# Performance work log

Hardware: AMD Instinct MI355X
Metric: run time of the kernel (lower is better)

## Reference

```python
import jax, jax.numpy as jnp
import numpy as np

N = 32768        # total nodes (B * max_num_nodes)
E = 524288       # edges, avg degree 16
F_ORI = 32       # data.x_ori feature dim
F_G = 32         # each gamora_output feature dim
IN = F_ORI + 3 * F_G  # 128
H = 256          # hidden_dim
OUT = 16         # out_dim
MAXN = 1024      # max_num_nodes
EPS = 1e-5       # BatchNorm eps


def setup_inputs() -> dict:
    key = jax.random.key(0)
    ks = list(jax.random.split(key, 32))
    g = lambda k, shape, fan: jax.random.normal(k, shape, jnp.float32) / np.sqrt(fan)
    inp = {}
    inp['x_ori'] = jax.random.normal(ks[0], (N, F_ORI), jnp.float32)
    inp['g0'] = jax.random.normal(ks[1], (N, F_G), jnp.float32)
    inp['g1'] = jax.random.normal(ks[2], (N, F_G), jnp.float32)
    inp['g2'] = jax.random.normal(ks[3], (N, F_G), jnp.float32)
    inp['edge_index'] = jax.random.randint(ks[4], (2, E), 0, N, jnp.int64)
    # SAGEConv layer 0: in_dim -> hidden
    inp['Wl0'] = g(ks[5], (IN, H), IN)
    inp['Wr0'] = g(ks[6], (IN, H), IN)
    inp['bb0'] = jnp.zeros((H,), jnp.float32)
    # SAGEConv layers 1..3: hidden -> hidden (stacked)
    inp['Wl'] = g(ks[7], (3, H, H), H)
    inp['Wr'] = g(ks[8], (3, H, H), H)
    inp['bb'] = jnp.zeros((3, H), jnp.float32)
    # BatchNorm per conv layer
    inp['gamma'] = jnp.ones((4, H), jnp.float32)
    inp['beta'] = jnp.zeros((4, H), jnp.float32)
    # mlp1: [max_num_nodes, hidden, 1]
    inp['W1a'] = g(ks[9], (MAXN, H), MAXN)
    inp['b1a'] = jnp.zeros((H,), jnp.float32)
    inp['W1b'] = g(ks[10], (H, 1), H)
    inp['b1b'] = jnp.zeros((1,), jnp.float32)
    # final BatchNorm
    inp['gamma_f'] = jnp.ones((H,), jnp.float32)
    inp['beta_f'] = jnp.zeros((H,), jnp.float32)
    # mlp2: [hidden, hidden, out_dim]
    inp['W2a'] = g(ks[11], (H, H), H)
    inp['b2a'] = jnp.zeros((H,), jnp.float32)
    inp['W2b'] = g(ks[12], (H, OUT), H)
    inp['b2b'] = jnp.zeros((OUT,), jnp.float32)
    return inp


def _bn(x, gamma, beta):
    # training-mode BatchNorm1d over the node/batch axis (biased variance)
    m = jnp.mean(x, axis=0)
    v = jnp.var(x, axis=0)
    return (x - m) * jax.lax.rsqrt(v + EPS) * gamma + beta


def _sage(x, src, dst, inv_deg, Wl, Wr, b):
    # mean neighbor aggregation (gather -> segment_sum -> normalize), then
    # out = lin_l(mean_agg) + lin_r(x)  (PyG SAGEConv, aggr='mean')
    agg = jax.ops.segment_sum(x[src], dst, num_segments=N)
    mean = agg * inv_deg[:, None]
    return mean @ Wl + x @ Wr + b


def reference(x_ori, g0, g1, g2, edge_index, Wl0, Wr0, bb0, Wl, Wr, bb,
              gamma, beta, W1a, b1a, W1b, b1b, gamma_f, beta_f,
              W2a, b2a, W2b, b2b):
    x = jnp.concatenate([x_ori, g0, g1, g2], axis=1)  # [N, IN]
    dst, src = edge_index[0], edge_index[1]
    deg = jax.ops.segment_sum(jnp.ones((E,), x.dtype), dst, num_segments=N)
    inv_deg = jnp.where(deg > 0, 1.0 / jnp.maximum(deg, 1.0), 0.0)
    # layer 0
    x = jax.nn.relu(_bn(_sage(x, src, dst, inv_deg, Wl0, Wr0, bb0), gamma[0], beta[0]))
    # layers 1..3 (dropout is identity in eval-mode reference)
    for i in range(3):
        x = jax.nn.relu(_bn(_sage(x, src, dst, inv_deg, Wl[i], Wr[i], bb[i]),
                            gamma[i + 1], beta[i + 1]))
    x = x.reshape(-1, H, MAXN)                 # [B, H, MAXN]
    h = jax.nn.relu(x @ W1a + b1a)             # [B, H, H]
    x = (h @ W1b + b1b).squeeze(2)             # [B, H]
    x = jax.nn.relu(_bn(x, gamma_f, beta_f))
    x = jax.nn.relu(x @ W2a + b2a) @ W2b + b2b  # [B, OUT]
    return x
```

## Files before the change

kernel.cpp:

```cpp
#include <hip/hip_runtime.h>

#define NN 32768
#define NE 524288
#define HD 256
#define TOTP 794897

#define GAS __attribute__((address_space(1)))
#define LAS __attribute__((address_space(3)))

typedef __attribute__((ext_vector_type(8))) __bf16 bf16x8;
typedef __attribute__((ext_vector_type(4))) float f32x4;

__device__ __forceinline__ float ld_any(const void* p, int i, int isbf16) {
    return isbf16 ? (float)((const __bf16*)p)[i] : ((const float*)p)[i];
}

struct PtrTable { const void* p[18]; };


__global__ __launch_bounds__(256) void k_pre(const unsigned* __restrict__ xw, const int* __restrict__ ei,
                                             PtrTable pt, const void* __restrict__ p0, const void* __restrict__ p1,
                                             const void* __restrict__ p2, const void* __restrict__ p3,
                                             int* __restrict__ flags, int* __restrict__ deg,
                                             __bf16* __restrict__ blob, __bf16* __restrict__ X0c) {
    __shared__ int fl[2];
    const int t = threadIdx.x;
    if (t < 64) {
        unsigned L = xw[t] & 0xFFFFu;
        int e = (int)((L >> 7) & 0xFF);
        unsigned long long b = __ballot(e >= 90 && e <= 135);
        if (t == 0) fl[0] = (b == ~0ULL) ? 1 : 0;
    } else if (t < 128) {
        int u = t - 64;
        unsigned long long b = __ballot(ei[2 * u + 1] != 0);
        if (t == 64) fl[1] = (b == 0ULL) ? 1 : 0;
    }
    __syncthreads();
    const int f0 = fl[0], f1 = fl[1];
    const int blk = blockIdx.x;
    if (blk == 0 && t < 2) flags[t] = fl[t];
    if (blk < 2048) {
        int i0 = (blk * 256 + t) * 8;
        int n = i0 >> 7, f = i0 & 127;
        const void* src = (f < 32) ? p0 : (f < 64) ? p1 : (f < 96) ? p2 : p3;
        int si = n * 32 + (f & 31);
        bf16x8 o;
        #pragma unroll
        for (int j = 0; j < 8; ++j) o[j] = (__bf16)ld_any(src, si + j, f0);
        *(bf16x8*)&X0c[i0] = o;
    } else if (blk < 3601) {
        const int off[23] = {0, 32768, 65536, 65792, 131328, 196864, 262400, 327936, 393472,
                             459008, 459776, 460800, 461824, 723968, 724224, 724480, 724481,
                             724737, 724993, 790529, 790785, 794881, TOTP};
        const signed char pidx[22] = {0, 1, 2, 3, 3, 3, 4, 4, 4, 5, 6, 7, 8, 9, 10, 11, 12, 13, 14, 15, 16, 17};
        const int sbase[22] = {0, 0, 0, 0, 65536, 131072, 0, 65536, 131072, 0, 0, 0, 0, 0, 0, 0, 0, 0, 0, 0, 0, 0};
        const signed char lR[22] = {7, 7, -1, 8, 8, 8, 8, 8, 8, -1, -1, -1, 10, -1, -1, -1, -1, -1, -1, -1, -1, -1};
        const signed char lC[22] = {8, 8, 0, 8, 8, 8, 8, 8, 8, 0, 0, 0, 8, 0, 0, 0, 0, 0, 0, 0, 0, 0};
        int base = ((blk - 2048) * 256 + t) * 2;
        #pragma unroll
        for (int j = 0; j < 2; ++j) {
            int i = base + j;
            if (i >= TOTP) break;
            int s = 0;
            while (i >= off[s + 1]) ++s;
            int jj = i - off[s];
            int si;
            if (lR[s] >= 0) {
                int Rm = (1 << lR[s]) - 1;
                si = sbase[s] + ((jj & Rm) << lC[s]) + (jj >> lR[s]);
            } else {
                si = sbase[s] + jj;
            }
            blob[i] = (__bf16)ld_any(pt.p[pidx[s]], si, f0);
        }
    } else {
        int e0 = ((blk - 3601) * 256 + t) * 2;
        int d0 = f1 ? ei[2 * e0] : ei[e0];
        int d1 = f1 ? ei[2 * e0 + 2] : ei[e0 + 1];
        atomicAdd(&deg[d0], 1);
        atomicAdd(&deg[d1], 1);
    }
}


__global__ __launch_bounds__(256) void k_alloc(const int* __restrict__ deg, int* __restrict__ gcur,
                                               int* __restrict__ offs, float* __restrict__ invd) {
    const int n = blockIdx.x * 256 + threadIdx.x;
    const int lane = threadIdx.x & 63;
    const int v = deg[n];
    invd[n] = v ? 1.f / (float)v : 0.f;
    int incl = v;
    #pragma unroll
    for (int d = 1; d < 64; d <<= 1) {
        int y = __shfl_up(incl, d, 64);
        if (lane >= d) incl += y;
    }
    int base = 0;
    if (lane == 63) base = atomicAdd(gcur, incl);
    base = __shfl(base, 63, 64);
    offs[n] = base + incl - v;
}

__global__ __launch_bounds__(256) void k_fill(const int* __restrict__ ei, const int* __restrict__ flags,
                                              const int* __restrict__ offs, int* __restrict__ cursor,
                                              int* __restrict__ csr) {
    int e = blockIdx.x * 256 + threadIdx.x;
    int f = flags[1];
    int d = f ? ei[2 * e] : ei[e];
    int s = f ? ei[2 * NE + 2 * e] : ei[NE + e];
    int p = atomicAdd(&cursor[d], 1);
    csr[offs[d] + p] = s;
}


__global__ __launch_bounds__(256) void k_agg0(const __bf16* __restrict__ X, const int* __restrict__ csr,
                                              const int* __restrict__ offs, const int* __restrict__ deg,
                                              const float* __restrict__ invd, __bf16* __restrict__ M) {
    const int t = threadIdx.x;
    const int s = blockIdx.x & 1;
    const int n = (blockIdx.x >> 1) * 32 + (t >> 3);
    const int fo = s * 64 + (t & 7) * 8;
    const int beg = offs[n], end = beg + deg[n];
    float a[8] = {};
    for (int e = beg; e < end; e += 8) {
        #pragma unroll
        for (int u = 0; u < 8; ++u) {
            int ee = e + u;
            int idx = csr[ee < end ? ee : end - 1] & (NN - 1);
            float mk = ee < end ? 1.f : 0.f;
            bf16x8 v = *(const bf16x8*)&X[(size_t)idx * 128 + fo];
            #pragma unroll
            for (int j = 0; j < 8; ++j) a[j] += mk * (float)v[j];
        }
    }
    const float id = invd[n];
    bf16x8 o;
    #pragma unroll
    for (int j = 0; j < 8; ++j) o[j] = (__bf16)(a[j] * id);
    *(bf16x8*)&M[(size_t)n * 128 + fo] = o;
}

__global__ __launch_bounds__(256) void k_aggq(const unsigned char* __restrict__ Xq, const int* __restrict__ csr,
                                              const int* __restrict__ offs, const int* __restrict__ deg,
                                              const float* __restrict__ invd, __bf16* __restrict__ M) {
    const int t = threadIdx.x;
    const int s = blockIdx.x & 1;
    const int n = (blockIdx.x >> 1) * 32 + (t >> 3);
    const int fo = s * 128 + (t & 7) * 16;
    const int beg = offs[n], end = beg + deg[n];
    unsigned ae0 = 0, ao0 = 0, ae1 = 0, ao1 = 0, ae2 = 0, ao2 = 0, ae3 = 0, ao3 = 0;
    for (int e = beg; e < end; e += 8) {
        #pragma unroll
        for (int u = 0; u < 8; ++u) {
            int ee = e + u;
            int idx = csr[ee < end ? ee : end - 1] & (NN - 1);
            uint4 v = *(const uint4*)&Xq[(size_t)idx * HD + fo];
            if (ee >= end) { v.x = 0u; v.y = 0u; v.z = 0u; v.w = 0u; }
            ae0 += v.x & 0x00FF00FFu; ao0 += (v.x >> 8) & 0x00FF00FFu;
            ae1 += v.y & 0x00FF00FFu; ao1 += (v.y >> 8) & 0x00FF00FFu;
            ae2 += v.z & 0x00FF00FFu; ao2 += (v.z >> 8) & 0x00FF00FFu;
            ae3 += v.w & 0x00FF00FFu; ao3 += (v.w >> 8) & 0x00FF00FFu;
        }
    }
    const float sc = invd[n] * 0.03125f;
    float a[16];
    a[0]  = (float)(ae0 & 0xFFFFu); a[1]  = (float)(ao0 & 0xFFFFu);
    a[2]  = (float)(ae0 >> 16);     a[3]  = (float)(ao0 >> 16);
    a[4]  = (float)(ae1 & 0xFFFFu); a[5]  = (float)(ao1 & 0xFFFFu);
    a[6]  = (float)(ae1 >> 16);     a[7]  = (float)(ao1 >> 16);
    a[8]  = (float)(ae2 & 0xFFFFu); a[9]  = (float)(ao2 & 0xFFFFu);
    a[10] = (float)(ae2 >> 16);     a[11] = (float)(ao2 >> 16);
    a[12] = (float)(ae3 & 0xFFFFu); a[13] = (float)(ao3 & 0xFFFFu);
    a[14] = (float)(ae3 >> 16);     a[15] = (float)(ao3 >> 16);
    bf16x8 o0, o1;
    #pragma unroll
    for (int j = 0; j < 8; ++j) { o0[j] = (__bf16)(a[j] * sc); o1[j] = (__bf16)(a[8 + j] * sc); }
    *(bf16x8*)&M[(size_t)n * HD + fo] = o0;
    *(bf16x8*)&M[(size_t)n * HD + fo + 8] = o1;
}


template <int MODE, int TM, int BNA, int NP, int TN = 128>
__global__ __launch_bounds__(256) void k_gemm(const __bf16* __restrict__ A1, const __bf16* __restrict__ WT1,
                                              const __bf16* __restrict__ A2, const __bf16* __restrict__ WT2,
                                              const __bf16* __restrict__ bias, int KD,
                                              __bf16* __restrict__ O, float* __restrict__ colsum,
                                              const __bf16* __restrict__ W1b, float* __restrict__ x2,
                                              const float* __restrict__ pstatA, const __bf16* __restrict__ gA,
                                              const __bf16* __restrict__ bA) {
    constexpr int NWM = (TN == 128) ? 2 : 4;
    constexpr int MI = TM / (NWM * 16);
    __shared__ __bf16 As[NP][2][TM][32];
    __shared__ __bf16 Bs[NP][2][TN][32];
    __shared__ float scs[256], shs[256];
    const int t = threadIdx.x;
    const int lane = t & 63, w = t >> 6;
    const int wm = (TN == 128) ? (w >> 1) : w;
    const int wn = (TN == 128) ? (w & 1) : 0;
    const int quad = lane >> 4, l15 = lane & 15;
    const int row0 = blockIdx.x * TM, c0 = blockIdx.y * TN;
    const int dr = lane >> 2, dc = (lane & 3) * 8;
    if constexpr (BNA != 0) {
        const float invn = 1.0f / NN;
        float m = pstatA[t] * invn;
        float var = fmaxf(pstatA[256 + t] * invn - m * m, 0.f);
        float rs = rsqrtf(var + 1e-5f);
        float g = (float)gA[t] * rs;
        scs[t] = g;
        shs[t] = (float)bA[t] - m * g;
    }
    f32x4 acc[MI][4] = {};
    for (int k0 = 0; k0 < KD; k0 += 64) {
        __syncthreads();
        #pragma unroll
        for (int pass = 0; pass < NP; ++pass) {
            const __bf16* __restrict__ A = pass ? A2 : A1;
            const __bf16* __restrict__ WT = pass ? WT2 : WT1;
            #pragma unroll
            for (int kk = 0; kk < 2; ++kk) {
                #pragma unroll
                for (int i = 0; i < TN / 64; ++i) {
                    const __bf16* g = &WT[(size_t)(c0 + w * (TN / 4) + i * 16 + dr) * KD + k0 + kk * 32 + dc];
                    __builtin_amdgcn_global_load_lds((const GAS void*)g,
                                                     (LAS void*)&Bs[pass][kk][w * (TN / 4) + i * 16][0], 16, 0, 0);
                }
                if ((BNA >> pass) & 1) {
                    const int kb = (k0 + kk * 32 + dc) & 255;
                    #pragma unroll
                    for (int i = 0; i < TM / 64; ++i) {
                        const __bf16* g = &A[(size_t)(row0 + w * (TM / 4) + i * 16 + dr) * KD + k0 + kk * 32 + dc];
                        bf16x8 v = *(const bf16x8*)g;
                        bf16x8 o;
                        #pragma unroll
                        for (int j = 0; j < 8; ++j)
                            o[j] = (__bf16)fmaxf((float)v[j] * scs[kb + j] + shs[kb + j], 0.f);
                        *(bf16x8*)&As[pass][kk][w * (TM / 4) + i * 16 + dr][dc] = o;
                    }
                } else {
                    #pragma unroll
                    for (int i = 0; i < TM / 64; ++i) {
                        const __bf16* g = &A[(size_t)(row0 + w * (TM / 4) + i * 16 + dr) * KD + k0 + kk * 32 + dc];
                        __builtin_amdgcn_global_load_lds((const GAS void*)g,
                                                         (LAS void*)&As[pass][kk][w * (TM / 4) + i * 16][0],
                                                         16, 0, 0);
                    }
                }
            }
        }
        __syncthreads();
        #pragma unroll
        for (int pass = 0; pass < NP; ++pass) {
            #pragma unroll
            for (int kk = 0; kk < 2; ++kk) {
                bf16x8 af[MI], bfr[4];
                #pragma unroll
                for (int i = 0; i < MI; ++i)
                    af[i] = *(const bf16x8*)&As[pass][kk][wm * (TM / NWM) + i * 16 + l15][quad * 8];
                #pragma unroll
                for (int j = 0; j < 4; ++j)
                    bfr[j] = *(const bf16x8*)&Bs[pass][kk][wn * 64 + j * 16 + l15][quad * 8];
                #pragma unroll
                for (int i = 0; i < MI; ++i)
                    #pragma unroll
                    for (int j = 0; j < 4; ++j)
                        acc[i][j] = __builtin_amdgcn_mfma_f32_16x16x32_bf16(af[i], bfr[j], acc[i][j], 0, 0, 0);
            }
        }
    }
    __syncthreads();
    if constexpr (MODE == 0) {
        float* lsum = (float*)&As[0][0][0][0];
        lsum[t] = 0.f;
        __syncthreads();
        #pragma unroll
        for (int j = 0; j < 4; ++j) {
            const int cb = wn * 64 + j * 16 + l15;
            const int col = c0 + cb;
            const float b = (float)bias[col];
            float s = 0.f, q = 0.f;
            #pragma unroll
            for (int i = 0; i < MI; ++i) {
                const size_t rbase = (size_t)(row0 + wm * (TM / NWM) + i * 16 + quad * 4) * HD + col;
                #pragma unroll
                for (int r = 0; r < 4; ++r) {
                    float y = acc[i][j][r] + b;
                    O[rbase + (size_t)r * HD] = (__bf16)y;
                    s += y;
                    q += y * y;
                }
            }
            s += __shfl_xor(s, 16, 64); s += __shfl_xor(s, 32, 64);
            q += __shfl_xor(q, 16, 64); q += __shfl_xor(q, 32, 64);
            if (quad == 0) {
                atomicAdd(&lsum[cb], s);
                atomicAdd(&lsum[128 + cb], q);
            }
        }
        __syncthreads();
        if (t < 128) atomicAdd(&colsum[c0 + t], lsum[t]);
        else atomicAdd(&colsum[256 + c0 + t - 128], lsum[t]);
    } else {
        float bj[4], wj[4];
        #pragma unroll
        for (int j = 0; j < 4; ++j) {
            const int col = c0 + wn * 64 + j * 16 + l15;
            bj[j] = (float)bias[col];
            wj[j] = (float)W1b[col];
        }
        #pragma unroll
        for (int i = 0; i < MI; ++i) {
            #pragma unroll
            for (int r = 0; r < 4; ++r) {
                float p = 0.f;
                #pragma unroll
                for (int j = 0; j < 4; ++j) p += fmaxf(acc[i][j][r] + bj[j], 0.f) * wj[j];
                p += __shfl_xor(p, 1, 64); p += __shfl_xor(p, 2, 64);
                p += __shfl_xor(p, 4, 64); p += __shfl_xor(p, 8, 64);
                if (l15 == 0) atomicAdd(&x2[row0 + wm * (TM / NWM) + i * 16 + quad * 4 + r], p);
            }
        }
    }
}


__global__ __launch_bounds__(256) void k_bnapply(__bf16* __restrict__ Y, const float* __restrict__ pstat,
                                                 const __bf16* __restrict__ gamma, const __bf16* __restrict__ beta,
                                                 unsigned char* __restrict__ Xq) {
    __shared__ float sc[256], sh[256];
    const int t = threadIdx.x;
    {
        const float invn = 1.0f / NN;
        float m = pstat[t] * invn;
        float var = fmaxf(pstat[256 + t] * invn - m * m, 0.f);
        float rs = rsqrtf(var + 1e-5f);
        float s = (float)gamma[t] * rs;
        sc[t] = s;
        sh[t] = (float)beta[t] - m * s;
    }
    __syncthreads();
    size_t i = ((size_t)blockIdx.x * 256 + t) * 8;
    int c = (int)(i & 255);
    bf16x8 y = *(const bf16x8*)&Y[i];
    float yv[8];
    bf16x8 o;
    #pragma unroll
    for (int j = 0; j < 8; ++j) {
        float v = fmaxf((float)y[j] * sc[c + j] + sh[c + j], 0.f);
        yv[j] = v;
        o[j] = (__bf16)v;
    }
    *(bf16x8*)&Y[i] = o;
    unsigned q[8];
    #pragma unroll
    for (int j = 0; j < 8; ++j) q[j] = __float2uint_rn(fminf(yv[j], 7.96875f) * 32.f);
    unsigned w0 = q[0] | (q[1] << 8) | (q[2] << 16) | (q[3] << 24);
    unsigned w1 = q[4] | (q[5] << 8) | (q[6] << 16) | (q[7] << 24);
    uint2 pk; pk.x = w0; pk.y = w1;
    *(uint2*)&Xq[i] = pk;
}


__global__ __launch_bounds__(256) void k_mlp2(const float* __restrict__ x2, const __bf16* __restrict__ b1b,
                                              const __bf16* __restrict__ gf, const __bf16* __restrict__ bf_,
                                              const __bf16* __restrict__ W2a, const __bf16* __restrict__ b2a,
                                              const __bf16* __restrict__ W2b, const __bf16* __restrict__ b2b,
                                              const int* __restrict__ flags, void* __restrict__ out) {
    __shared__ float row[HD];
    __shared__ float hbuf[HD];
    __shared__ float part[256];
    const int b = blockIdx.x, t = threadIdx.x;
    const float b1 = (float)b1b[0];
    float s = 0.f, q = 0.f, mine = 0.f;
    #pragma unroll
    for (int r = 0; r < 32; ++r) {
        float v = x2[r * HD + t] + b1;
        s += v; q += v * v;
        if (r == b) mine = v;
    }
    float m = s * (1.0f / 32.0f);
    float var = fmaxf(q * (1.0f / 32.0f) - m * m, 0.f);
    float rs = rsqrtf(var + 1e-5f);
    float sc = (float)gf[t] * rs;
    float sh = (float)bf_[t] - m * sc;
    row[t] = fmaxf(mine * sc + sh, 0.f);
    __syncthreads();
    float acc = (float)b2a[t];
    for (int j = 0; j < HD; ++j) acc += row[j] * (float)W2a[j * HD + t];
    hbuf[t] = fmaxf(acc, 0.f);
    __syncthreads();
    const int k = t & 15, g = t >> 4;
    float p = 0.f;
    #pragma unroll
    for (int jj = 0; jj < 16; ++jj) p += hbuf[g * 16 + jj] * (float)W2b[(g * 16 + jj) * 16 + k];
    part[t] = p;
    __syncthreads();
    if (t < 16) {
        float o = (float)b2b[t];
        #pragma unroll
        for (int g2 = 0; g2 < 16; ++g2) o += part[g2 * 16 + t];
        if (flags[0]) ((__bf16*)out)[b * 16 + t] = (__bf16)o;
        else ((float*)out)[b * 16 + t] = o;
    }
}


extern "C" void kernel_launch(void* const* d_in, const int* in_sizes, int n_in,
                              void* d_out, int out_size, void* d_ws, size_t ws_size,
                              hipStream_t stream) {
    const int* ei = (const int*)d_in[4];

    char* ws = (char*)d_ws;
    size_t off_ = 0;
    auto ALLOC = [&](size_t b) { char* p = ws + off_; off_ += (b + 255) & ~(size_t)255; return p; };
    int* flags_ = (int*)ALLOC(8);
    size_t zbeg = off_;
    int* deg_ = (int*)ALLOC(NN * 4);
    int* cursor_ = (int*)ALLOC(NN * 4);
    float* colsum_ = (float*)ALLOC(4 * 512 * 4);
    float* x2_ = (float*)ALLOC(8192 * 4);
    int* gcur_ = (int*)ALLOC(4);
    size_t zlen = off_ - zbeg;
    int* offs_ = (int*)ALLOC(NN * 4);
    float* invd_ = (float*)ALLOC(NN * 4);
    int* csr_ = (int*)ALLOC((size_t)NE * 4);
    __bf16* blob_ = (__bf16*)ALLOC((size_t)TOTP * 2);
    unsigned char* Xq_ = (unsigned char*)ALLOC((size_t)NN * HD);
    __bf16* M_ = (__bf16*)ALLOC((size_t)NN * HD * 2);
    __bf16* Xa_ = (__bf16*)ALLOC((size_t)NN * HD * 2);
    __bf16* Xb_ = (__bf16*)ALLOC((size_t)NN * HD * 2);
    __bf16* X0c_ = Xb_;

    __bf16* Wl0T = blob_ + 0;
    __bf16* Wr0T = blob_ + 32768;
    __bf16* bb0c = blob_ + 65536;
    __bf16* WlT = blob_ + 65792;
    __bf16* WrT = blob_ + 262400;
    __bf16* bbc = blob_ + 459008;
    __bf16* gammac = blob_ + 459776;
    __bf16* betac = blob_ + 460800;
    __bf16* W1aT = blob_ + 461824;
    __bf16* b1ac = blob_ + 723968;
    __bf16* W1bc = blob_ + 724224;
    __bf16* b1bc = blob_ + 724480;
    __bf16* gfc = blob_ + 724481;
    __bf16* bfc = blob_ + 724737;
    __bf16* W2ac = blob_ + 724993;
    __bf16* b2ac = blob_ + 790529;
    __bf16* W2bc = blob_ + 790785;
    __bf16* b2bc = blob_ + 794881;

    PtrTable pt;
    pt.p[0] = d_in[5];  pt.p[1] = d_in[6];  pt.p[2] = d_in[7];  pt.p[3] = d_in[8];
    pt.p[4] = d_in[9];  pt.p[5] = d_in[10]; pt.p[6] = d_in[11]; pt.p[7] = d_in[12];
    pt.p[8] = d_in[13]; pt.p[9] = d_in[14]; pt.p[10] = d_in[15]; pt.p[11] = d_in[16];
    pt.p[12] = d_in[17]; pt.p[13] = d_in[18]; pt.p[14] = d_in[19]; pt.p[15] = d_in[20];
    pt.p[16] = d_in[21]; pt.p[17] = d_in[22];

    hipMemsetAsync(ws + zbeg, 0, zlen, stream);
    k_pre<<<4625, 256, 0, stream>>>((const unsigned*)d_in[0], ei, pt, d_in[0], d_in[1], d_in[2], d_in[3],
                                    flags_, deg_, blob_, X0c_);
    k_alloc<<<NN / 256, 256, 0, stream>>>(deg_, gcur_, offs_, invd_);
    k_fill<<<NE / 256, 256, 0, stream>>>(ei, flags_, offs_, cursor_, csr_);

    k_agg0<<<NN / 32 * 2, 256, 0, stream>>>(X0c_, csr_, offs_, deg_, invd_, M_);
    k_gemm<0, 128, 0, 2><<<dim3(NN / 128, 2), 256, 0, stream>>>(M_, Wl0T, X0c_, Wr0T, bb0c, 128, Xa_, colsum_,
                                                                nullptr, nullptr, nullptr, nullptr, nullptr);
    k_bnapply<<<NN / 8, 256, 0, stream>>>(Xa_, colsum_, gammac, betac, Xq_);

    __bf16* Xin = Xa_;
    __bf16* Xo = Xb_;
    for (int l = 0; l < 3; ++l) {
        float* cs = colsum_ + (l + 1) * 512;
        k_aggq<<<NN / 32 * 2, 256, 0, stream>>>(Xq_, csr_, offs_, deg_, invd_, M_);
        k_gemm<0, 128, 0, 2><<<dim3(NN / 128, 2), 256, 0, stream>>>(M_, WlT + (size_t)l * HD * HD, Xin,
                                                                    WrT + (size_t)l * HD * HD, bbc + l * HD, 256,
                                                                    Xo, cs, nullptr, nullptr, nullptr, nullptr,
                                                                    nullptr);
        if (l < 2) k_bnapply<<<NN / 8, 256, 0, stream>>>(Xo, cs, gammac + (l + 1) * HD, betac + (l + 1) * HD, Xq_);
        __bf16* tmp = Xin; Xin = Xo; Xo = tmp;
    }

    k_gemm<1, 64, 1, 1, 64><<<dim3(8192 / 64, 4), 256, 0, stream>>>(Xin, W1aT, nullptr, nullptr, b1ac, 1024,
                                                                    nullptr, nullptr, W1bc, x2_,
                                                                    colsum_ + 3 * 512, gammac + 3 * HD,
                                                                    betac + 3 * HD);
    k_mlp2<<<32, 256, 0, stream>>>(x2_, b1bc, gfc, bfc, W2ac, b2ac, W2bc, b2bc, flags_, d_out);
}
```

Baseline: 409.4 us.

## Double-buffer SAGE GEMM K-loop with async LDS loads and vmcnt waits

Restructures the MODE 0 GEMM used by the SAGE layers into a two-stage software pipeline. The next K-step's global-to-LDS loads are issued before computing the current one, with s_waitcnt vmcnt and raw barriers instead of full __syncthreads. Both the lin_l and lin_r passes are flattened into one step sequence. This is meant to hide global load latency behind MFMA work. The MLP1 GEMM path instead becomes a sequential per-pass loop, and correctness depends on the hand-counted vmcnt(8) matching the number of outstanding loads.

```diff
diff --git a/kernel.cpp b/kernel.cpp
--- a/kernel.cpp
+++ b/kernel.cpp
@@ -180,7 +180,7 @@
 }
 
 
-template <int MODE, int TM, int BNA, int NP, int TN = 128>
+template <int MODE, int TM, int BNA, int TN = 128>
 __global__ __launch_bounds__(256) void k_gemm(const __bf16* __restrict__ A1, const __bf16* __restrict__ WT1,
                                               const __bf16* __restrict__ A2, const __bf16* __restrict__ WT2,
                                               const __bf16* __restrict__ bias, int KD,
@@ -190,8 +190,8 @@
                                               const __bf16* __restrict__ bA) {
     constexpr int NWM = (TN == 128) ? 2 : 4;
     constexpr int MI = TM / (NWM * 16);
-    __shared__ __bf16 As[NP][2][TM][32];
-    __shared__ __bf16 Bs[NP][2][TN][32];
+    __shared__ __bf16 As[2][2][TM][32];
+    __shared__ __bf16 Bs[2][2][TN][32];
     __shared__ float scs[256], shs[256];
     const int t = threadIdx.x;
     const int lane = t & 63, w = t >> 6;
@@ -210,60 +210,112 @@
         shs[t] = (float)bA[t] - m * g;
     }
     f32x4 acc[MI][4] = {};
-    for (int k0 = 0; k0 < KD; k0 += 64) {
-        __syncthreads();
-        #pragma unroll
-        for (int pass = 0; pass < NP; ++pass) {
-            const __bf16* __restrict__ A = pass ? A2 : A1;
-            const __bf16* __restrict__ WT = pass ? WT2 : WT1;
+    const int npass = A2 ? 2 : 1;
+
+    if constexpr (MODE == 0 && BNA == 0) {
+        const int KS = KD / 64;
+        const int NSTEPS = npass * KS;
+        auto stage = [&](int s, int b) {
+            const int p = (s >= KS) ? 1 : 0;
+            const __bf16* __restrict__ A = p ? A2 : A1;
+            const __bf16* __restrict__ WT = p ? WT2 : WT1;
+            const int k0 = (s - p * KS) * 64;
             #pragma unroll
             for (int kk = 0; kk < 2; ++kk) {
                 #pragma unroll
                 for (int i = 0; i < TN / 64; ++i) {
                     const __bf16* g = &WT[(size_t)(c0 + w * (TN / 4) + i * 16 + dr) * KD + k0 + kk * 32 + dc];
                     __builtin_amdgcn_global_load_lds((const GAS void*)g,
-                                                     (LAS void*)&Bs[pass][kk][w * (TN / 4) + i * 16][0], 16, 0, 0);
+                                                     (LAS void*)&Bs[b][kk][w * (TN / 4) + i * 16][0], 16, 0, 0);
                 }
-                if ((BNA >> pass) & 1) {
-                    const int kb = (k0 + kk * 32 + dc) & 255;
-                    #pragma unroll
-                    for (int i = 0; i < TM / 64; ++i) {
-                        const __bf16* g = &A[(size_t)(row0 + w * (TM / 4) + i * 16 + dr) * KD + k0 + kk * 32 + dc];
-                        bf16x8 v = *(const bf16x8*)g;
-                        bf16x8 o;
-                        #pragma unroll
-                        for (int j = 0; j < 8; ++j)
-                            o[j] = (__bf16)fmaxf((float)v[j] * scs[kb + j] + shs[kb + j], 0.f);
-                        *(bf16x8*)&As[pass][kk][w * (TM / 4) + i * 16 + dr][dc] = o;
-                    }
-                } else {
-                    #pragma unroll
-                    for (int i = 0; i < TM / 64; ++i) {
-                        const __bf16* g = &A[(size_t)(row0 + w * (TM / 4) + i * 16 + dr) * KD + k0 + kk * 32 + dc];
-                        __builtin_amdgcn_global_load_lds((const GAS void*)g,
-                                                         (LAS void*)&As[pass][kk][w * (TM / 4) + i * 16][0],
-                                                         16, 0, 0);
-                    }
+                #pragma unroll
+                for (int i = 0; i < TM / 64; ++i) {
+                    const __bf16* g = &A[(size_t)(row0 + w * (TM / 4) + i * 16 + dr) * KD + k0 + kk * 32 + dc];
+                    __builtin_amdgcn_global_load_lds((const GAS void*)g,
+                                                     (LAS void*)&As[b][kk][w * (TM / 4) + i * 16][0], 16, 0, 0);
                 }
             }
-        }
-        __syncthreads();
-        #pragma unroll
-        for (int pass = 0; pass < NP; ++pass) {
+        };
+        stage(0, 0);
+        int cur = 0;
+        for (int s = 0; s < NSTEPS; ++s) {
+            if (s + 1 < NSTEPS) {
+                stage(s + 1, cur ^ 1);
+                asm volatile("s_waitcnt vmcnt(8)" ::: "memory");
+            } else {
+                asm volatile("s_waitcnt vmcnt(0)" ::: "memory");
+            }
+            asm volatile("s_barrier" ::: "memory");
             #pragma unroll
             for (int kk = 0; kk < 2; ++kk) {
                 bf16x8 af[MI], bfr[4];
                 #pragma unroll
                 for (int i = 0; i < MI; ++i)
-                    af[i] = *(const bf16x8*)&As[pass][kk][wm * (TM / NWM) + i * 16 + l15][quad * 8];
+                    af[i] = *(const bf16x8*)&As[cur][kk][wm * (TM / NWM) + i * 16 + l15][quad * 8];
                 #pragma unroll
                 for (int j = 0; j < 4; ++j)
-                    bfr[j] = *(const bf16x8*)&Bs[pass][kk][wn * 64 + j * 16 + l15][quad * 8];
+                    bfr[j] = *(const bf16x8*)&Bs[cur][kk][wn * 64 + j * 16 + l15][quad * 8];
                 #pragma unroll
                 for (int i = 0; i < MI; ++i)
                     #pragma unroll
                     for (int j = 0; j < 4; ++j)
                         acc[i][j] = __builtin_amdgcn_mfma_f32_16x16x32_bf16(af[i], bfr[j], acc[i][j], 0, 0, 0);
+            }
+            asm volatile("s_barrier" ::: "memory");
+            cur ^= 1;
+        }
+    } else {
+        for (int pass = 0; pass < npass; ++pass) {
+            const __bf16* __restrict__ A = pass ? A2 : A1;
+            const __bf16* __restrict__ WT = pass ? WT2 : WT1;
+            for (int k0 = 0; k0 < KD; k0 += 64) {
+                __syncthreads();
+                #pragma unroll
+                for (int kk = 0; kk < 2; ++kk) {
+                    #pragma unroll
+                    for (int i = 0; i < TN / 64; ++i) {
+                        const __bf16* g = &WT[(size_t)(c0 + w * (TN / 4) + i * 16 + dr) * KD + k0 + kk * 32 + dc];
+                        __builtin_amdgcn_global_load_lds((const GAS void*)g,
+                                                         (LAS void*)&Bs[0][kk][w * (TN / 4) + i * 16][0], 16, 0, 0);
+                    }
+                    if ((BNA >> pass) & 1) {
+                        const int kb = (k0 + kk * 32 + dc) & 255;
+                        #pragma unroll
+                        for (int i = 0; i < TM / 64; ++i) {
+                            const __bf16* g = &A[(size_t)(row0 + w * (TM / 4) + i * 16 + dr) * KD + k0 + kk * 32 + dc];
+                            bf16x8 v = *(const bf16x8*)g;
+                            bf16x8 o;
+                            #pragma unroll
+                            for (int j = 0; j < 8; ++j)
+                                o[j] = (__bf16)fmaxf((float)v[j] * scs[kb + j] + shs[kb + j], 0.f);
+                            *(bf16x8*)&As[0][kk][w * (TM / 4) + i * 16 + dr][dc] = o;
+                        }
+                    } else {
+                        #pragma unroll
+                        for (int i = 0; i < TM / 64; ++i) {
+                            const __bf16* g = &A[(size_t)(row0 + w * (TM / 4) + i * 16 + dr) * KD + k0 + kk * 32 + dc];
+                            __builtin_amdgcn_global_load_lds((const GAS void*)g,
+                                                             (LAS void*)&As[0][kk][w * (TM / 4) + i * 16][0],
+                                                             16, 0, 0);
+                        }
+                    }
+                }
+                __syncthreads();
+                #pragma unroll
+                for (int kk = 0; kk < 2; ++kk) {
+                    bf16x8 af[MI], bfr[4];
+                    #pragma unroll
+                    for (int i = 0; i < MI; ++i)
+                        af[i] = *(const bf16x8*)&As[0][kk][wm * (TM / NWM) + i * 16 + l15][quad * 8];
+                    #pragma unroll
+                    for (int j = 0; j < 4; ++j)
+                        bfr[j] = *(const bf16x8*)&Bs[0][kk][wn * 64 + j * 16 + l15][quad * 8];
+                    #pragma unroll
+                    for (int i = 0; i < MI; ++i)
+                        #pragma unroll
+                        for (int j = 0; j < 4; ++j)
+                            acc[i][j] = __builtin_amdgcn_mfma_f32_16x16x32_bf16(af[i], bfr[j], acc[i][j], 0, 0, 0);
+                }
             }
         }
     }
@@ -463,8 +515,8 @@
     k_fill<<<NE / 256, 256, 0, stream>>>(ei, flags_, offs_, cursor_, csr_);
 
     k_agg0<<<NN / 32 * 2, 256, 0, stream>>>(X0c_, csr_, offs_, deg_, invd_, M_);
-    k_gemm<0, 128, 0, 2><<<dim3(NN / 128, 2), 256, 0, stream>>>(M_, Wl0T, X0c_, Wr0T, bb0c, 128, Xa_, colsum_,
-                                                                nullptr, nullptr, nullptr, nullptr, nullptr);
+    k_gemm<0, 128, 0><<<dim3(NN / 128, 2), 256, 0, stream>>>(M_, Wl0T, X0c_, Wr0T, bb0c, 128, Xa_, colsum_,
+                                                             nullptr, nullptr, nullptr, nullptr, nullptr);
     k_bnapply<<<NN / 8, 256, 0, stream>>>(Xa_, colsum_, gammac, betac, Xq_);
 
     __bf16* Xin = Xa_;
@@ -472,17 +524,17 @@
     for (int l = 0; l < 3; ++l) {
         float* cs = colsum_ + (l + 1) * 512;
         k_aggq<<<NN / 32 * 2, 256, 0, stream>>>(Xq_, csr_, offs_, deg_, invd_, M_);
-        k_gemm<0, 128, 0, 2><<<dim3(NN / 128, 2), 256, 0, stream>>>(M_, WlT + (size_t)l * HD * HD, Xin,
-                                                                    WrT + (size_t)l * HD * HD, bbc + l * HD, 256,
-                                                                    Xo, cs, nullptr, nullptr, nullptr, nullptr,
-                                                                    nullptr);
+        k_gemm<0, 128, 0><<<dim3(NN / 128, 2), 256, 0, stream>>>(M_, WlT + (size_t)l * HD * HD, Xin,
+                                                                 WrT + (size_t)l * HD * HD, bbc + l * HD, 256,
+                                                                 Xo, cs, nullptr, nullptr, nullptr, nullptr,
+                                                                 nullptr);
         if (l < 2) k_bnapply<<<NN / 8, 256, 0, stream>>>(Xo, cs, gammac + (l + 1) * HD, betac + (l + 1) * HD, Xq_);
         __bf16* tmp = Xin; Xin = Xo; Xo = tmp;
     }
 
-    k_gemm<1, 64, 1, 1, 64><<<dim3(8192 / 64, 4), 256, 0, stream>>>(Xin, W1aT, nullptr, nullptr, b1ac, 1024,
-                                                                    nullptr, nullptr, W1bc, x2_,
-                                                                    colsum_ + 3 * 512, gammac + 3 * HD,
-                                                                    betac + 3 * HD);
+    k_gemm<1, 64, 1, 64><<<dim3(8192 / 64, 4), 256, 0, stream>>>(Xin, W1aT, nullptr, nullptr, b1ac, 1024,
+                                                                 nullptr, nullptr, W1bc, x2_,
+                                                                 colsum_ + 3 * 512, gammac + 3 * HD,
+                                                                 betac + 3 * HD);
     k_mlp2<<<32, 256, 0, stream>>>(x2_, b1bc, gfc, bfc, W2ac, b2ac, W2bc, b2bc, flags_, d_out);
 }
```

New measurement: 407.1 us. Within noise of the previous version (-0.6%).
